# Kernel tuning notes

Hardware: AMD Instinct MI355X
Metric: run time of the kernel (lower is better)

The kernel has to match this reference:

```python
import jax, jax.numpy as jnp
import numpy as np

T, B, F, L = 512, 4096, 16, 4  # seq_len, batch, input_size, n_layers; hidden_size H = 1


def _lstm_layer(seq, W_ih, W_hh, b_ih, b_hh):
    """Single unidirectional LSTM layer, H=1.
    seq: [T, B, in]; W_ih: [4, in]; W_hh: [4, 1]; b_ih, b_hh: [4].
    Returns (hs [T,B,1], h_T [B,1], c_T [B,1]). Gate order i,f,g,o (PyTorch).
    """
    # Input contribution for all timesteps at once (the only sizeable GEMM).
    gx = jnp.einsum('tbi,gi->tbg', seq, W_ih) + b_ih + b_hh  # [T, B, 4]
    Bb = seq.shape[1]
    h0 = jnp.zeros((Bb, 1), seq.dtype)
    c0 = jnp.zeros((Bb, 1), seq.dtype)

    def step(carry, g):
        h, c = carry
        gates = g + h @ W_hh.T  # [B, 4]
        i = jax.nn.sigmoid(gates[:, 0:1])
        f = jax.nn.sigmoid(gates[:, 1:2])
        gg = jnp.tanh(gates[:, 2:3])
        o = jax.nn.sigmoid(gates[:, 3:4])
        c = f * c + i * gg
        h = o * jnp.tanh(c)
        return (h, c), h

    (hT, cT), hs = jax.lax.scan(step, (h0, c0), gx)
    return hs, hT, cT


def setup_inputs() -> dict:
    key = jax.random.key(0)
    ks = jax.random.split(key, 6)
    s = 0.5  # ~U(-1,1) stdev scale; 1/sqrt(H)=1 in torch init
    return {
        'x': jax.random.normal(ks[0], (T, B, F), jnp.float32),
        'W_ih0': jax.random.normal(ks[1], (4, F), jnp.float32) * s,
        'W_ih_rest': jax.random.normal(ks[2], (L - 1, 4, 1), jnp.float32) * s,
        'W_hh': jax.random.normal(ks[3], (L, 4, 1), jnp.float32) * s,
        'b_ih': jax.random.normal(ks[4], (L, 4), jnp.float32) * s,
        'b_hh': jax.random.normal(ks[5], (L, 4), jnp.float32) * s,
    }


def reference(x, W_ih0, W_ih_rest, W_hh, b_ih, b_hh):
    seq = x
    hns, cns = [], []
    for l in range(L):
        W_ih_l = W_ih0 if l == 0 else W_ih_rest[l - 1]
        seq, hT, cT = _lstm_layer(seq, W_ih_l, W_hh[l], b_ih[l], b_hh[l])
        hns.append(hT)
        cns.append(cT)
    output = seq                      # [T, B, 1] last-layer hidden sequence
    hn = jnp.stack(hns, axis=0)       # [L, B, 1]
    cn = jnp.stack(cns, axis=0)       # [L, B, 1]
    return output, hn, cn
```

## Files before the change

### kernel.cpp

```cpp
#include <hip/hip_runtime.h>

#define T_DIM 512
#define B_DIM 4096
#define L_DIM 4
#define LOG2E 1.44269504088896f

typedef float f4 __attribute__((ext_vector_type(4)));

template <int CTRL>
__device__ __forceinline__ float dpp_mov(float v) {
  int r = __builtin_amdgcn_update_dpp(0, __builtin_bit_cast(int, v), CTRL, 0xf, 0xf, true);
  return __builtin_bit_cast(float, r);
}
template <int CTRL>
__device__ __forceinline__ float qp_add(float v) { return v + dpp_mov<CTRL>(v); }

__device__ __forceinline__ void ld_f4(f4& dst, unsigned voff, const f4* base) {
  asm volatile("global_load_dwordx4 %0, %1, %2"
               : "=v"(dst) : "v"(voff), "s"(base) : "memory");
}
__device__ __forceinline__ void wait_ring(f4* buf) {
  asm volatile("s_waitcnt vmcnt(0)"
               : "+v"(buf[0]), "+v"(buf[1]), "+v"(buf[2]), "+v"(buf[3]),
                 "+v"(buf[4]), "+v"(buf[5]), "+v"(buf[6]), "+v"(buf[7])
               :: "memory");
}

__global__ __launch_bounds__(64, 1) void lstm_fused(
    const float* __restrict__ x,
    const float* __restrict__ Wih0,
    const float* __restrict__ Wrest,
    const float* __restrict__ Whh,
    const float* __restrict__ bih, const float* __restrict__ bhh,
    float* __restrict__ out) {
  const int lane = threadIdx.x;
  const int g = lane & 3;
  const int l = (lane >> 2) & 3;
  const int c = (lane >> 4) & 3;
  const int chain = blockIdx.x * 4 + c;
  const bool l0 = (l == 0);

  const float sgo[4] = {-LOG2E, -LOG2E, 2.0f * LOG2E, -LOG2E};

  const float whh  = sgo[g] * Whh[l * 4 + g];
  const float wih  = l0 ? 0.f : sgo[g] * Wrest[(l - 1) * 4 + g];
  const float base = l0 ? 0.f : sgo[g] * (bih[l * 4 + g] + bhh[l * 4 + g]);
  f4 wx;
  {
    const f4 wv = ((const f4*)Wih0)[l * 4 + g];
    const float s = sgo[l];
    wx.x = s * wv.x; wx.y = s * wv.y; wx.z = s * wv.z; wx.w = s * wv.w;
  }
  const float dinit = (g == 0) ? sgo[l] * (bih[l] + bhh[l]) : 0.f;
  const float vm = (g == 2) ? -2.f : 1.f;
  const float va = (g == 2) ? 1.f : 0.f;
  const int bperm_addr = 4 * ((lane & 0x30) | (g << 2));

  float* __restrict__ po = out + chain;
  float h = 0.f, cs = 0.f;
  float hsv[8];

  const char* xb = (const char*)x + (size_t)blockIdx.x * 256;
  unsigned vj[8];
#pragma unroll
  for (int j = 0; j < 8; ++j)
    vj[j] = (unsigned)(c * 64 + g * 16) + (unsigned)j * 262144u;

  f4 A[8], Bq[8];

  auto load8 = [&](f4* buf, int t0) {
    const f4* p = (const f4*)(xb + (size_t)t0 * 262144);
#pragma unroll
    for (int j = 0; j < 8; ++j) ld_f4(buf[j], vj[j], p);
  };

  auto cell = [&](int k, int j, f4 xv, bool guard) {
    float p = fmaf(xv.x, wx.x, fmaf(xv.y, wx.y, fmaf(xv.z, wx.z, fmaf(xv.w, wx.w, dinit))));
    p = qp_add<0xB1>(p);
    p = qp_add<0x4E>(p);
    float D = __builtin_bit_cast(float,
        __builtin_amdgcn_ds_bpermute(bperm_addr, __builtin_bit_cast(int, p)));

    float hin = dpp_mov<0x114>(h);
    float pb = l0 ? D : base;
    float gate = fmaf(whh, h, fmaf(wih, hin, pb));

    float r = __builtin_amdgcn_rcpf(1.0f + __builtin_amdgcn_exp2f(gate));
    float v = fmaf(vm, r, va);

    float f_ = dpp_mov<0x55>(v);
    float tg = dpp_mov<0xAA>(v);
    float o_ = dpp_mov<0xFF>(v);
    float cn = fmaf(f_, cs, v * tg);
    float tcn = fmaf(-2.0f,
        __builtin_amdgcn_rcpf(1.0f + __builtin_amdgcn_exp2f(2.88539008178f * cn)), 1.0f);
    float hm = o_ * tcn;
    float hn = dpp_mov<0x00>(hm);

    if (guard) {
      const int t = k - l;
      const bool valid = (unsigned)t < (unsigned)T_DIM;
      cs = valid ? cn : cs;
      h  = valid ? hn : h;
    } else {
      cs = cn; h = hn;
    }
    hsv[j] = hn;
  };
  auto cells8 = [&](int k0, f4* buf, bool guard) {
#pragma unroll
    for (int j = 0; j < 8; ++j) cell(k0 + j, j, buf[j], guard);
  };
  auto flush = [&](int k0, int jlo, int jhi) {
    if (l == 3 && g == 0) {
#pragma unroll
      for (int j = 0; j < 8; ++j)
        if (j >= jlo && j <= jhi) po[(size_t)(k0 + j - 3) * B_DIM] = hsv[j];
    }
  };

  load8(A, 0);
  wait_ring(A);
  load8(Bq, 8);
  cells8(0, A, true);
  wait_ring(Bq); flush(0, 3, 7);  load8(A, 16);  cells8(8, Bq, false);
  wait_ring(A);  flush(8, 0, 7);  load8(Bq, 24); cells8(16, A, false);
#pragma unroll 1
  for (int n = 3; n < 63; n += 2) {
    wait_ring(Bq); flush(8 * (n - 1), 0, 7); load8(A, 8 * (n + 1));
    cells8(8 * n, Bq, false);
    wait_ring(A);  flush(8 * n, 0, 7);       load8(Bq, 8 * (n + 2));
    cells8(8 * (n + 1), A, false);
  }
  wait_ring(Bq); flush(8 * 62, 0, 7);
  cells8(504, Bq, false);
  flush(504, 0, 7);
  cells8(512, Bq, true);
  flush(512, 0, 2);

  if (g == 0) {
    po[(size_t)T_DIM * B_DIM + (size_t)l * B_DIM] = h;
    po[(size_t)T_DIM * B_DIM + (size_t)L_DIM * B_DIM + (size_t)l * B_DIM] = cs;
  }
}

extern "C" void kernel_launch(void* const* d_in, const int* in_sizes, int n_in,
                              void* d_out, int out_size, void* d_ws, size_t ws_size,
                              hipStream_t stream) {
  const float* x     = (const float*)d_in[0];
  const float* Wih0  = (const float*)d_in[1];
  const float* Wrest = (const float*)d_in[2];
  const float* Whh   = (const float*)d_in[3];
  const float* bih   = (const float*)d_in[4];
  const float* bhh   = (const float*)d_in[5];
  float* out = (float*)d_out;
  lstm_fused<<<B_DIM / 4, 64, 0, stream>>>(x, Wih0, Wrest, Whh, bih, bhh, out);
}
```

Measured before the change: 245.1 us.

## Remap input-projection lanes to drop bpermute and hoist dot products off recurrence

```diff
diff --git a/kernel.cpp b/kernel.cpp
--- a/kernel.cpp
+++ b/kernel.cpp
@@ -47,14 +47,13 @@
   const float base = l0 ? 0.f : sgo[g] * (bih[l * 4 + g] + bhh[l * 4 + g]);
   f4 wx;
   {
-    const f4 wv = ((const f4*)Wih0)[l * 4 + g];
-    const float s = sgo[l];
+    const f4 wv = ((const f4*)Wih0)[g * 4 + l];
+    const float s = sgo[g];
     wx.x = s * wv.x; wx.y = s * wv.y; wx.z = s * wv.z; wx.w = s * wv.w;
   }
-  const float dinit = (g == 0) ? sgo[l] * (bih[l] + bhh[l]) : 0.f;
+  const float dinit = l0 ? sgo[g] * (bih[g] + bhh[g]) : 0.f;
   const float vm = (g == 2) ? -2.f : 1.f;
   const float va = (g == 2) ? 1.f : 0.f;
-  const int bperm_addr = 4 * ((lane & 0x30) | (g << 2));
 
   float* __restrict__ po = out + chain;
   float h = 0.f, cs = 0.f;
@@ -64,7 +63,7 @@
   unsigned vj[8];
 #pragma unroll
   for (int j = 0; j < 8; ++j)
-    vj[j] = (unsigned)(c * 64 + g * 16) + (unsigned)j * 262144u;
+    vj[j] = (unsigned)(c * 64 + l * 16) + (unsigned)j * 262144u;
 
   f4 A[8], Bq[8];
 
@@ -74,13 +73,7 @@
     for (int j = 0; j < 8; ++j) ld_f4(buf[j], vj[j], p);
   };
 
-  auto cell = [&](int k, int j, f4 xv, bool guard) {
-    float p = fmaf(xv.x, wx.x, fmaf(xv.y, wx.y, fmaf(xv.z, wx.z, fmaf(xv.w, wx.w, dinit))));
-    p = qp_add<0xB1>(p);
-    p = qp_add<0x4E>(p);
-    float D = __builtin_bit_cast(float,
-        __builtin_amdgcn_ds_bpermute(bperm_addr, __builtin_bit_cast(int, p)));
-
+  auto cell = [&](int k, int j, float D, bool guard) {
     float hin = dpp_mov<0x114>(h);
     float pb = l0 ? D : base;
     float gate = fmaf(whh, h, fmaf(wih, hin, pb));
@@ -88,28 +81,38 @@
     float r = __builtin_amdgcn_rcpf(1.0f + __builtin_amdgcn_exp2f(gate));
     float v = fmaf(vm, r, va);
 
+    float i_ = dpp_mov<0x00>(v);
     float f_ = dpp_mov<0x55>(v);
     float tg = dpp_mov<0xAA>(v);
     float o_ = dpp_mov<0xFF>(v);
-    float cn = fmaf(f_, cs, v * tg);
+    float cn = fmaf(f_, cs, i_ * tg);
     float tcn = fmaf(-2.0f,
         __builtin_amdgcn_rcpf(1.0f + __builtin_amdgcn_exp2f(2.88539008178f * cn)), 1.0f);
     float hm = o_ * tcn;
-    float hn = dpp_mov<0x00>(hm);
 
     if (guard) {
       const int t = k - l;
       const bool valid = (unsigned)t < (unsigned)T_DIM;
       cs = valid ? cn : cs;
-      h  = valid ? hn : h;
+      h  = valid ? hm : h;
     } else {
-      cs = cn; h = hn;
+      cs = cn; h = hm;
     }
-    hsv[j] = hn;
+    hsv[j] = hm;
   };
+
   auto cells8 = [&](int k0, f4* buf, bool guard) {
+    float D[8];
 #pragma unroll
-    for (int j = 0; j < 8; ++j) cell(k0 + j, j, buf[j], guard);
+    for (int j = 0; j < 8; ++j) {
+      const f4 xv = buf[j];
+      float p = fmaf(xv.x, wx.x, fmaf(xv.y, wx.y, fmaf(xv.z, wx.z, fmaf(xv.w, wx.w, dinit))));
+      p = qp_add<0x124>(p);
+      p = qp_add<0x128>(p);
+      D[j] = p;
+    }
+#pragma unroll
+    for (int j = 0; j < 8; ++j) cell(k0 + j, j, D[j], guard);
   };
   auto flush = [&](int k0, int jlo, int jhi) {
     if (l == 3 && g == 0) {
```

Measured after the change: 238.8 us. 2.6% less time.
